# Performance work log

Hardware: AMD Instinct MI355X
Metric: run time of the kernel (lower is better)

The kernel has to match this reference:

```python
import jax, jax.numpy as jnp
import numpy as np

NUM_HEADS = 12
HEAD_DIM = 64
DIM = 768
ATTN_DIM = 768
SEQ = 4096


def _rotate_half(t):
    # split last dim in halves: (x1, x2) -> (-x2, x1)
    x1, x2 = jnp.split(t, 2, axis=-1)
    return jnp.concatenate([-x2, x1], axis=-1)


def _apply_rope(t, freqs):
    # t: [B,H,L,d], freqs: [1,1,L,d]
    return t * jnp.cos(freqs) + _rotate_half(t) * jnp.sin(freqs)


def setup_inputs() -> dict:
    key = jax.random.key(0)
    ks = jax.random.split(key, 8)
    x = jax.random.normal(ks[0], (1, SEQ, DIM), dtype=jnp.float32)
    # standard rotary frequencies: theta = pos * inv_freq, concatenated twice to head_dim
    inv_freq = 1.0 / (10000.0 ** (jnp.arange(0, HEAD_DIM, 2, dtype=jnp.float32) / HEAD_DIM))
    pos = jnp.arange(SEQ, dtype=jnp.float32)
    ang = pos[:, None] * inv_freq[None, :]                      # [L, d/2]
    rope = jnp.concatenate([ang, ang], axis=-1)[None, None]     # [1,1,L,d]
    s = 0.02
    Wq = jax.random.normal(ks[1], (ATTN_DIM, DIM), dtype=jnp.float32) * s
    Wk = jax.random.normal(ks[2], (ATTN_DIM, DIM), dtype=jnp.float32) * s
    Wv = jax.random.normal(ks[3], (ATTN_DIM, DIM), dtype=jnp.float32) * s
    Wo = jax.random.normal(ks[4], (DIM, ATTN_DIM), dtype=jnp.float32) * s
    bo = jnp.zeros((DIM,), dtype=jnp.float32)
    gamma = jnp.ones((DIM,), dtype=jnp.float32)
    beta = jnp.zeros((DIM,), dtype=jnp.float32)
    return {"x": x, "Wq": Wq, "Wk": Wk, "Wv": Wv, "Wo": Wo, "bo": bo,
            "gamma": gamma, "beta": beta, "rope": rope}


def reference(x, Wq, Wk, Wv, Wo, bo, gamma, beta, rope):
    B, L, D = x.shape
    residual = x
    # pre-LayerNorm
    mu = jnp.mean(x, axis=-1, keepdims=True)
    var = jnp.mean((x - mu) ** 2, axis=-1, keepdims=True)
    xn = (x - mu) * jax.lax.rsqrt(var + 1e-5) * gamma + beta

    def heads(t):  # [B,L,attn_dim] -> [B,H,L,d]
        return t.reshape(B, L, NUM_HEADS, HEAD_DIM).transpose(0, 2, 1, 3)

    q = heads(xn @ Wq.T)
    k = heads(xn @ Wk.T)
    v = heads(xn @ Wv.T)
    q = _apply_rope(q, rope)
    k = _apply_rope(k, rope)
    v = _apply_rope(v, rope)

    scale = HEAD_DIM ** -0.5
    dots = jnp.einsum('bhid,bhjd->bhij', q, k) * scale
    # causal mask: positions j > i masked
    i = jnp.arange(L)
    mask = i[:, None] < i[None, :]  # True where future
    neg = -jnp.finfo(dots.dtype).max
    dots = jnp.where(mask[None, None], neg, dots)
    attn_map = jax.nn.softmax(dots, axis=-1)

    o = jnp.einsum('bhij,bhjd->bhid', attn_map, v)
    o = o.transpose(0, 2, 1, 3).reshape(B, L, ATTN_DIM)
    out = o @ Wo.T + bo + residual
    return out, attn_map, dots
```

## Files before the change

### kernel.cpp

```cpp
#include <hip/hip_runtime.h>
#include <hip/hip_bf16.h>
#include <cfloat>
#include <cmath>

#define SEQ 4096
#define DIM 768
#define NH 12
#define HD 64
#define NEG_MASK (-0x1.FEp+127f)

typedef __attribute__((ext_vector_type(8))) short short8_t;
typedef __attribute__((ext_vector_type(4))) float f32x4;

static __device__ __forceinline__ unsigned short f2bf(float f) {
  __hip_bfloat16 h = __float2bfloat16(f);
  unsigned short u;
  __builtin_memcpy(&u, &h, 2);
  return u;
}

__global__ __launch_bounds__(256) void ln_kernel(const float* __restrict__ x,
    const float* __restrict__ gamma, const float* __restrict__ beta,
    unsigned short* __restrict__ xnb) {
  int row = blockIdx.x;
  const float* xr = x + (size_t)row * DIM;
  int t = threadIdx.x;
  float v0 = xr[t], v1 = xr[t + 256], v2 = xr[t + 512];
  float s = v0 + v1 + v2;
  float s2 = v0 * v0 + v1 * v1 + v2 * v2;
  for (int off = 32; off > 0; off >>= 1) {
    s += __shfl_down(s, off, 64);
    s2 += __shfl_down(s2, off, 64);
  }
  __shared__ float red[2][4];
  int wid = t >> 6;
  if ((t & 63) == 0) { red[0][wid] = s; red[1][wid] = s2; }
  __syncthreads();
  s = red[0][0] + red[0][1] + red[0][2] + red[0][3];
  s2 = red[1][0] + red[1][1] + red[1][2] + red[1][3];
  float mu = s * (1.0f / DIM);
  float var = s2 * (1.0f / DIM) - mu * mu;
  float rstd = rsqrtf(var + 1e-5f);
  unsigned short* xo = xnb + (size_t)row * DIM;
  xo[t]       = f2bf((v0 - mu) * rstd * gamma[t]       + beta[t]);
  xo[t + 256] = f2bf((v1 - mu) * rstd * gamma[t + 256] + beta[t + 256]);
  xo[t + 512] = f2bf((v2 - mu) * rstd * gamma[t + 512] + beta[t + 512]);
}

__global__ __launch_bounds__(256) void wcvt_kernel(const float* __restrict__ w0,
    const float* __restrict__ w1, const float* __restrict__ w2, const float* __restrict__ w3,
    unsigned short* __restrict__ o0, unsigned short* __restrict__ o1,
    unsigned short* __restrict__ o2, unsigned short* __restrict__ o3) {
  const float* src; unsigned short* dst;
  switch (blockIdx.y) {
    case 0: src = w0; dst = o0; break;
    case 1: src = w1; dst = o1; break;
    case 2: src = w2; dst = o2; break;
    default: src = w3; dst = o3; break;
  }
  size_t base = ((size_t)blockIdx.x * 256 + threadIdx.x) * 8;
  float4 a = *(const float4*)(src + base);
  float4 b = *(const float4*)(src + base + 4);
  ushort4 ua, ub;
  ua.x = f2bf(a.x); ua.y = f2bf(a.y); ua.z = f2bf(a.z); ua.w = f2bf(a.w);
  ub.x = f2bf(b.x); ub.y = f2bf(b.y); ub.z = f2bf(b.z); ub.w = f2bf(b.w);
  *(ushort4*)(dst + base) = ua;
  *(ushort4*)(dst + base + 4) = ub;
}

__global__ __launch_bounds__(256) void qkv_kernel(const unsigned short* __restrict__ xnb,
    const unsigned short* __restrict__ wqb, const unsigned short* __restrict__ wkb,
    const unsigned short* __restrict__ wvb, const float* __restrict__ ropes,
    unsigned short* __restrict__ qb, unsigned short* __restrict__ kb,
    unsigned short* __restrict__ vbT) {
  int z = blockIdx.z;
  const unsigned short* W = (z == 0) ? wqb : (z == 1) ? wkb : wvb;
  int h = blockIdx.y;
  int n0 = h * 64;
  int tid = threadIdx.x;
  int w = tid >> 6, l = tid & 63;
  int col_l = l & 15, rowg = l >> 4, kgrp = rowg * 8;
  int mbase = blockIdx.x * 64 + w * 16;

  f32x4 acc[4];
  #pragma unroll
  for (int g = 0; g < 4; g++) acc[g] = (f32x4){0.f, 0.f, 0.f, 0.f};

  for (int k0 = 0; k0 < DIM; k0 += 32) {
    short8_t a = *(const short8_t*)(xnb + (size_t)(mbase + col_l) * DIM + k0 + kgrp);
    #pragma unroll
    for (int g = 0; g < 4; g++) {
      short8_t bw = *(const short8_t*)(W + (size_t)(n0 + g * 16 + col_l) * DIM + k0 + kgrp);
      acc[g] = __builtin_amdgcn_mfma_f32_16x16x32_bf16(a, bw, acc[g], 0, 0, 0);
    }
  }

  float res[4][4];
  #pragma unroll
  for (int g = 0; g < 4; g++) {
    int d = g * 16 + col_l;
    #pragma unroll
    for (int r = 0; r < 4; r++) {
      int m = mbase + rowg * 4 + r;
      float f = ropes[(size_t)m * HD + d];
      float val = acc[g][r];
      float oth = acc[g ^ 2][r];
      float rot = (g < 2) ? -oth : oth;
      res[g][r] = val * cosf(f) + rot * sinf(f);
    }
  }

  if (z < 2) {
    unsigned short* dst = (z == 0) ? qb : kb;
    #pragma unroll
    for (int g = 0; g < 4; g++) {
      int d = g * 16 + col_l;
      #pragma unroll
      for (int r = 0; r < 4; r++)
        dst[((size_t)h * SEQ + mbase + rowg * 4 + r) * HD + d] = f2bf(res[g][r]);
    }
  } else {
    #pragma unroll
    for (int g = 0; g < 4; g++) {
      int d = g * 16 + col_l;
      ushort4 u;
      u.x = f2bf(res[g][0]); u.y = f2bf(res[g][1]);
      u.z = f2bf(res[g][2]); u.w = f2bf(res[g][3]);
      *(ushort4*)(vbT + ((size_t)h * HD + d) * SEQ + mbase + rowg * 4) = u;
    }
  }
}

__global__ __launch_bounds__(256) void attn_fused(
    const unsigned short* __restrict__ qb, const unsigned short* __restrict__ kb,
    const unsigned short* __restrict__ vbT,
    float* __restrict__ dots, float* __restrict__ attnp, unsigned short* __restrict__ ob) {
  int band = blockIdx.x;
  int h = blockIdx.y;
  int i0 = band * 16;
  int jd = i0 >> 6;
  int tid = threadIdx.x;
  int w = tid >> 6, l = tid & 63;
  int col_l = l & 15, rg = l >> 4, kgrp = rg * 8;
  int c4 = col_l * 4;

  const unsigned short* qh = qb + (size_t)h * SEQ * HD;
  const unsigned short* kh = kb + (size_t)h * SEQ * HD;
  const unsigned short* vh = vbT + (size_t)h * HD * SEQ;
  size_t obase = (size_t)h * SEQ * SEQ;

  __shared__ float pt[4][16][68];
  __shared__ float stats[4][16][2];

  const unsigned short* qrow = qh + (size_t)(i0 + col_l) * HD + kgrp;
  short8_t aq0 = *(const short8_t*)(qrow);
  short8_t aq1 = *(const short8_t*)(qrow + 32);

  float mreg[4], lreg[4];
  #pragma unroll
  for (int r = 0; r < 4; r++) { mreg[r] = -FLT_MAX; lreg[r] = 0.f; }

  short8_t ka0[4], ka1[4];
  if (w <= jd) {
    #pragma unroll
    for (int b = 0; b < 4; b++) {
      const unsigned short* kr = kh + (size_t)(w * 64 + b * 16 + col_l) * HD + kgrp;
      ka0[b] = *(const short8_t*)(kr);
      ka1[b] = *(const short8_t*)(kr + 32);
    }
  }
  for (int jt = w; jt <= jd; jt += 4) {
    int j0 = jt * 64;
    bool hasNext = (jt + 4 <= jd);
    short8_t kb0[4], kb1[4];
    if (hasNext) {
      #pragma unroll
      for (int b = 0; b < 4; b++) {
        const unsigned short* kr = kh + (size_t)(j0 + 256 + b * 16 + col_l) * HD + kgrp;
        kb0[b] = *(const short8_t*)(kr);
        kb1[b] = *(const short8_t*)(kr + 32);
      }
    }
    f32x4 acc[4];
    #pragma unroll
    for (int b = 0; b < 4; b++) {
      f32x4 z = {0.f, 0.f, 0.f, 0.f};
      acc[b] = __builtin_amdgcn_mfma_f32_16x16x32_bf16(aq0, ka0[b], z, 0, 0, 0);
      acc[b] = __builtin_amdgcn_mfma_f32_16x16x32_bf16(aq1, ka1[b], acc[b], 0, 0, 0);
    }
    bool diag = (jt == jd);
    #pragma unroll
    for (int b = 0; b < 4; b++) {
      int j = j0 + b * 16 + col_l;
      #pragma unroll
      for (int r = 0; r < 4; r++) {
        float s = acc[b][r] * 0.125f;
        acc[b][r] = (diag && j > i0 + rg * 4 + r) ? NEG_MASK : s;
      }
    }
    #pragma unroll
    for (int r = 0; r < 4; r++) {
      float tm = fmaxf(fmaxf(acc[0][r], acc[1][r]), fmaxf(acc[2][r], acc[3][r]));
      if (tm > -1e30f) {
        float nm = fmaxf(mreg[r], tm);
        lreg[r] = lreg[r] * __expf(mreg[r] - nm) +
                  __expf(acc[0][r] - nm) + __expf(acc[1][r] - nm) +
                  __expf(acc[2][r] - nm) + __expf(acc[3][r] - nm);
        mreg[r] = nm;
      }
    }
    #pragma unroll
    for (int b = 0; b < 4; b++)
      #pragma unroll
      for (int r = 0; r < 4; r++)
        pt[w][rg * 4 + r][b * 16 + col_l] = acc[b][r];
    #pragma unroll
    for (int e = 0; e < 4; e++) {
      float4 v = *(const float4*)&pt[w][e * 4 + rg][c4];
      *(float4*)(dots + obase + (size_t)(i0 + e * 4 + rg) * SEQ + j0 + c4) = v;
    }
    if (hasNext) {
      #pragma unroll
      for (int b = 0; b < 4; b++) { ka0[b] = kb0[b]; ka1[b] = kb1[b]; }
    }
  }

  #pragma unroll
  for (int r = 0; r < 4; r++) {
    float m = mreg[r], lv = lreg[r];
    #pragma unroll
    for (int off = 1; off < 16; off <<= 1) {
      float om = __shfl_xor(m, off, 16);
      float ol = __shfl_xor(lv, off, 16);
      float nm = fmaxf(m, om);
      lv = lv * __expf(m - nm) + ol * __expf(om - nm);
      m = nm;
    }
    mreg[r] = m; lreg[r] = lv;
  }
  if (col_l == 0) {
    #pragma unroll
    for (int r = 0; r < 4; r++) {
      stats[w][rg * 4 + r][0] = mreg[r];
      stats[w][rg * 4 + r][1] = lreg[r];
    }
  }
  __syncthreads();
  float M_[4], rl_[4];
  #pragma unroll
  for (int r = 0; r < 4; r++) {
    int row = rg * 4 + r;
    float m0 = stats[0][row][0], m1 = stats[1][row][0];
    float m2 = stats[2][row][0], m3 = stats[3][row][0];
    float mm = fmaxf(fmaxf(m0, m1), fmaxf(m2, m3));
    float L = stats[0][row][1] * __expf(m0 - mm) + stats[1][row][1] * __expf(m1 - mm) +
              stats[2][row][1] * __expf(m2 - mm) + stats[3][row][1] * __expf(m3 - mm);
    M_[r] = mm;
    rl_[r] = 1.0f / L;
  }

  f32x4 o[4];
  #pragma unroll
  for (int dg = 0; dg < 4; dg++) o[dg] = (f32x4){0.f, 0.f, 0.f, 0.f};

  for (int jt = w; jt <= jd; jt += 4) {
    int j0 = jt * 64;
    short8_t bv0[4], bv1[4];
    #pragma unroll
    for (int dg = 0; dg < 4; dg++) {
      const unsigned short* vr = vh + (size_t)(dg * 16 + col_l) * SEQ + j0 + kgrp;
      bv0[dg] = *(const short8_t*)(vr);
      bv1[dg] = *(const short8_t*)(vr + 32);
    }
    f32x4 acc[4];
    #pragma unroll
    for (int b = 0; b < 4; b++) {
      const unsigned short* kr = kh + (size_t)(j0 + b * 16 + col_l) * HD + kgrp;
      short8_t bk0 = *(const short8_t*)(kr);
      short8_t bk1 = *(const short8_t*)(kr + 32);
      f32x4 z = {0.f, 0.f, 0.f, 0.f};
      acc[b] = __builtin_amdgcn_mfma_f32_16x16x32_bf16(aq0, bk0, z, 0, 0, 0);
      acc[b] = __builtin_amdgcn_mfma_f32_16x16x32_bf16(aq1, bk1, acc[b], 0, 0, 0);
    }
    bool diag = (jt == jd);
    #pragma unroll
    for (int b = 0; b < 4; b++) {
      int j = j0 + b * 16 + col_l;
      #pragma unroll
      for (int r = 0; r < 4; r++) {
        float s = acc[b][r] * 0.125f;
        s = (diag && j > i0 + rg * 4 + r) ? NEG_MASK : s;
        float p = __expf(s - M_[r]) * rl_[r];
        pt[w][rg * 4 + r][b * 16 + col_l] = p;
      }
    }
    #pragma unroll
    for (int e = 0; e < 4; e++) {
      float4 v = *(const float4*)&pt[w][e * 4 + rg][c4];
      *(float4*)(attnp + obase + (size_t)(i0 + e * 4 + rg) * SEQ + j0 + c4) = v;
    }
    short8_t pa[2];
    #pragma unroll
    for (int ks = 0; ks < 2; ks++) {
      const float* src = &pt[w][col_l][ks * 32 + kgrp];
      float4 x0 = *(const float4*)src;
      float4 x1 = *(const float4*)(src + 4);
      short8_t t;
      t[0] = (short)f2bf(x0.x); t[1] = (short)f2bf(x0.y);
      t[2] = (short)f2bf(x0.z); t[3] = (short)f2bf(x0.w);
      t[4] = (short)f2bf(x1.x); t[5] = (short)f2bf(x1.y);
      t[6] = (short)f2bf(x1.z); t[7] = (short)f2bf(x1.w);
      pa[ks] = t;
    }
    #pragma unroll
    for (int dg = 0; dg < 4; dg++) {
      o[dg] = __builtin_amdgcn_mfma_f32_16x16x32_bf16(pa[0], bv0[dg], o[dg], 0, 0, 0);
      o[dg] = __builtin_amdgcn_mfma_f32_16x16x32_bf16(pa[1], bv1[dg], o[dg], 0, 0, 0);
    }
  }

  {
    int c0 = (jd + 1) * 64;
    int nf4 = (SEQ - c0) >> 2;
    if (nf4 > 0) {
      float4 dm = make_float4(NEG_MASK, NEG_MASK, NEG_MASK, NEG_MASK);
      float4 zz = make_float4(0.f, 0.f, 0.f, 0.f);
      for (int r16 = 0; r16 < 16; r16++) {
        float4* dr = (float4*)(dots  + obase + (size_t)(i0 + r16) * SEQ + c0);
        float4* ar = (float4*)(attnp + obase + (size_t)(i0 + r16) * SEQ + c0);
        for (int c = tid; c < nf4; c += 256) { dr[c] = dm; ar[c] = zz; }
      }
    }
  }

  __syncthreads();
  #pragma unroll
  for (int dg = 0; dg < 4; dg++)
    #pragma unroll
    for (int r = 0; r < 4; r++)
      pt[w][rg * 4 + r][dg * 16 + col_l] = o[dg][r];
  __syncthreads();
  {
    int idx = tid * 4;
    int row = idx >> 6, col = idx & 63;
    float4 s = *(const float4*)&pt[0][row][col];
    #pragma unroll
    for (int w2 = 1; w2 < 4; w2++) {
      float4 t = *(const float4*)&pt[w2][row][col];
      s.x += t.x; s.y += t.y; s.z += t.z; s.w += t.w;
    }
    ushort4 u;
    u.x = f2bf(s.x); u.y = f2bf(s.y); u.z = f2bf(s.z); u.w = f2bf(s.w);
    *(ushort4*)(ob + (size_t)(i0 + row) * DIM + h * HD + col) = u;
  }
}

__global__ __launch_bounds__(256) void out_kernel(const unsigned short* __restrict__ ob,
    const unsigned short* __restrict__ wob, const float* __restrict__ bias,
    const float* __restrict__ resid, float* __restrict__ out) {
  int n0 = blockIdx.y * 64;
  int tid = threadIdx.x;
  int w = tid >> 6, l = tid & 63;
  int col_l = l & 15, rowg = l >> 4, kgrp = rowg * 8;
  int mbase = blockIdx.x * 64 + w * 16;

  f32x4 acc[4];
  #pragma unroll
  for (int g = 0; g < 4; g++) acc[g] = (f32x4){0.f, 0.f, 0.f, 0.f};

  for (int k0 = 0; k0 < DIM; k0 += 32) {
    short8_t a = *(const short8_t*)(ob + (size_t)(mbase + col_l) * DIM + k0 + kgrp);
    #pragma unroll
    for (int g = 0; g < 4; g++) {
      short8_t bw = *(const short8_t*)(wob + (size_t)(n0 + g * 16 + col_l) * DIM + k0 + kgrp);
      acc[g] = __builtin_amdgcn_mfma_f32_16x16x32_bf16(a, bw, acc[g], 0, 0, 0);
    }
  }
  #pragma unroll
  for (int g = 0; g < 4; g++) {
    int n = n0 + g * 16 + col_l;
    float bn = bias[n];
    #pragma unroll
    for (int r = 0; r < 4; r++) {
      int m = mbase + rowg * 4 + r;
      out[(size_t)m * DIM + n] = acc[g][r] + bn + resid[(size_t)m * DIM + n];
    }
  }
}

extern "C" void kernel_launch(void* const* d_in, const int* in_sizes, int n_in,
                              void* d_out, int out_size, void* d_ws, size_t ws_size,
                              hipStream_t stream) {
  const float* x     = (const float*)d_in[0];
  const float* Wq    = (const float*)d_in[1];
  const float* Wk    = (const float*)d_in[2];
  const float* Wv    = (const float*)d_in[3];
  const float* Wo    = (const float*)d_in[4];
  const float* bo    = (const float*)d_in[5];
  const float* gamma = (const float*)d_in[6];
  const float* beta  = (const float*)d_in[7];
  const float* rope  = (const float*)d_in[8];

  float* out  = (float*)d_out;
  float* attn = out + (size_t)SEQ * DIM;
  float* dots = attn + (size_t)NH * SEQ * SEQ;

  char* ws = (char*)d_ws;
  unsigned short* xnb = (unsigned short*)(ws);
  unsigned short* qb  = (unsigned short*)(ws + 6291456);
  unsigned short* kb  = (unsigned short*)(ws + 12582912);
  unsigned short* vbT = (unsigned short*)(ws + 18874368);
  unsigned short* ob  = (unsigned short*)(ws + 25165824);
  unsigned short* wqb = (unsigned short*)(ws + 31457280);
  unsigned short* wkb = (unsigned short*)(ws + 32636928);
  unsigned short* wvb = (unsigned short*)(ws + 33816576);
  unsigned short* wob = (unsigned short*)(ws + 34996224);

  ln_kernel<<<SEQ, 256, 0, stream>>>(x, gamma, beta, xnb);
  wcvt_kernel<<<dim3(288, 4), 256, 0, stream>>>(Wq, Wk, Wv, Wo, wqb, wkb, wvb, wob);
  qkv_kernel<<<dim3(SEQ / 64, NH, 3), 256, 0, stream>>>(xnb, wqb, wkb, wvb, rope, qb, kb, vbT);
  attn_fused<<<dim3(SEQ / 16, NH), 256, 0, stream>>>(qb, kb, vbT, dots, attn, ob);
  out_kernel<<<dim3(SEQ / 64, DIM / 64), 256, 0, stream>>>(ob, wob, bo, x, out);
}
```

Before: 594.4 us.

## Use nontemporal stores for attention outputs, reverse band order, drop K/V prefetch

```diff
diff --git a/kernel.cpp b/kernel.cpp
--- a/kernel.cpp
+++ b/kernel.cpp
@@ -17,6 +17,13 @@
   unsigned short u;
   __builtin_memcpy(&u, &h, 2);
   return u;
+}
+
+static __device__ __forceinline__ void st_nt(float* p, f32x4 v) {
+  __builtin_nontemporal_store(v, (f32x4*)p);
+}
+static __device__ __forceinline__ f32x4 ld_lds4(const float* p) {
+  return *(const f32x4*)p;
 }
 
 __global__ __launch_bounds__(256) void ln_kernel(const float* __restrict__ x,
@@ -131,11 +138,11 @@
   }
 }
 
-__global__ __launch_bounds__(256) void attn_fused(
+__global__ __launch_bounds__(256, 4) void attn_fused(
     const unsigned short* __restrict__ qb, const unsigned short* __restrict__ kb,
     const unsigned short* __restrict__ vbT,
     float* __restrict__ dots, float* __restrict__ attnp, unsigned short* __restrict__ ob) {
-  int band = blockIdx.x;
+  int band = (SEQ / 16 - 1) - blockIdx.x;
   int h = blockIdx.y;
   int i0 = band * 16;
   int jd = i0 >> 6;
@@ -160,33 +167,17 @@
   #pragma unroll
   for (int r = 0; r < 4; r++) { mreg[r] = -FLT_MAX; lreg[r] = 0.f; }
 
-  short8_t ka0[4], ka1[4];
-  if (w <= jd) {
-    #pragma unroll
-    for (int b = 0; b < 4; b++) {
-      const unsigned short* kr = kh + (size_t)(w * 64 + b * 16 + col_l) * HD + kgrp;
-      ka0[b] = *(const short8_t*)(kr);
-      ka1[b] = *(const short8_t*)(kr + 32);
-    }
-  }
   for (int jt = w; jt <= jd; jt += 4) {
     int j0 = jt * 64;
-    bool hasNext = (jt + 4 <= jd);
-    short8_t kb0[4], kb1[4];
-    if (hasNext) {
-      #pragma unroll
-      for (int b = 0; b < 4; b++) {
-        const unsigned short* kr = kh + (size_t)(j0 + 256 + b * 16 + col_l) * HD + kgrp;
-        kb0[b] = *(const short8_t*)(kr);
-        kb1[b] = *(const short8_t*)(kr + 32);
-      }
-    }
     f32x4 acc[4];
     #pragma unroll
     for (int b = 0; b < 4; b++) {
+      const unsigned short* kr = kh + (size_t)(j0 + b * 16 + col_l) * HD + kgrp;
+      short8_t bk0 = *(const short8_t*)(kr);
+      short8_t bk1 = *(const short8_t*)(kr + 32);
       f32x4 z = {0.f, 0.f, 0.f, 0.f};
-      acc[b] = __builtin_amdgcn_mfma_f32_16x16x32_bf16(aq0, ka0[b], z, 0, 0, 0);
-      acc[b] = __builtin_amdgcn_mfma_f32_16x16x32_bf16(aq1, ka1[b], acc[b], 0, 0, 0);
+      acc[b] = __builtin_amdgcn_mfma_f32_16x16x32_bf16(aq0, bk0, z, 0, 0, 0);
+      acc[b] = __builtin_amdgcn_mfma_f32_16x16x32_bf16(aq1, bk1, acc[b], 0, 0, 0);
     }
     bool diag = (jt == jd);
     #pragma unroll
@@ -216,12 +207,8 @@
         pt[w][rg * 4 + r][b * 16 + col_l] = acc[b][r];
     #pragma unroll
     for (int e = 0; e < 4; e++) {
-      float4 v = *(const float4*)&pt[w][e * 4 + rg][c4];
-      *(float4*)(dots + obase + (size_t)(i0 + e * 4 + rg) * SEQ + j0 + c4) = v;
-    }
-    if (hasNext) {
-      #pragma unroll
-      for (int b = 0; b < 4; b++) { ka0[b] = kb0[b]; ka1[b] = kb1[b]; }
+      f32x4 v = ld_lds4(&pt[w][e * 4 + rg][c4]);
+      st_nt(dots + obase + (size_t)(i0 + e * 4 + rg) * SEQ + j0 + c4, v);
     }
   }
 
@@ -265,13 +252,6 @@
 
   for (int jt = w; jt <= jd; jt += 4) {
     int j0 = jt * 64;
-    short8_t bv0[4], bv1[4];
-    #pragma unroll
-    for (int dg = 0; dg < 4; dg++) {
-      const unsigned short* vr = vh + (size_t)(dg * 16 + col_l) * SEQ + j0 + kgrp;
-      bv0[dg] = *(const short8_t*)(vr);
-      bv1[dg] = *(const short8_t*)(vr + 32);
-    }
     f32x4 acc[4];
     #pragma unroll
     for (int b = 0; b < 4; b++) {
@@ -296,15 +276,15 @@
     }
     #pragma unroll
     for (int e = 0; e < 4; e++) {
-      float4 v = *(const float4*)&pt[w][e * 4 + rg][c4];
-      *(float4*)(attnp + obase + (size_t)(i0 + e * 4 + rg) * SEQ + j0 + c4) = v;
+      f32x4 v = ld_lds4(&pt[w][e * 4 + rg][c4]);
+      st_nt(attnp + obase + (size_t)(i0 + e * 4 + rg) * SEQ + j0 + c4, v);
     }
     short8_t pa[2];
     #pragma unroll
     for (int ks = 0; ks < 2; ks++) {
       const float* src = &pt[w][col_l][ks * 32 + kgrp];
-      float4 x0 = *(const float4*)src;
-      float4 x1 = *(const float4*)(src + 4);
+      f32x4 x0 = ld_lds4(src);
+      f32x4 x1 = ld_lds4(src + 4);
       short8_t t;
       t[0] = (short)f2bf(x0.x); t[1] = (short)f2bf(x0.y);
       t[2] = (short)f2bf(x0.z); t[3] = (short)f2bf(x0.w);
@@ -314,8 +294,11 @@
     }
     #pragma unroll
     for (int dg = 0; dg < 4; dg++) {
-      o[dg] = __builtin_amdgcn_mfma_f32_16x16x32_bf16(pa[0], bv0[dg], o[dg], 0, 0, 0);
-      o[dg] = __builtin_amdgcn_mfma_f32_16x16x32_bf16(pa[1], bv1[dg], o[dg], 0, 0, 0);
+      const unsigned short* vr = vh + (size_t)(dg * 16 + col_l) * SEQ + j0 + kgrp;
+      short8_t bv0 = *(const short8_t*)(vr);
+      short8_t bv1 = *(const short8_t*)(vr + 32);
+      o[dg] = __builtin_amdgcn_mfma_f32_16x16x32_bf16(pa[0], bv0, o[dg], 0, 0, 0);
+      o[dg] = __builtin_amdgcn_mfma_f32_16x16x32_bf16(pa[1], bv1, o[dg], 0, 0, 0);
     }
   }
 
@@ -323,12 +306,15 @@
     int c0 = (jd + 1) * 64;
     int nf4 = (SEQ - c0) >> 2;
     if (nf4 > 0) {
-      float4 dm = make_float4(NEG_MASK, NEG_MASK, NEG_MASK, NEG_MASK);
-      float4 zz = make_float4(0.f, 0.f, 0.f, 0.f);
+      f32x4 dm = (f32x4){NEG_MASK, NEG_MASK, NEG_MASK, NEG_MASK};
+      f32x4 zz = (f32x4){0.f, 0.f, 0.f, 0.f};
       for (int r16 = 0; r16 < 16; r16++) {
-        float4* dr = (float4*)(dots  + obase + (size_t)(i0 + r16) * SEQ + c0);
-        float4* ar = (float4*)(attnp + obase + (size_t)(i0 + r16) * SEQ + c0);
-        for (int c = tid; c < nf4; c += 256) { dr[c] = dm; ar[c] = zz; }
+        float* dr = dots  + obase + (size_t)(i0 + r16) * SEQ + c0;
+        float* ar = attnp + obase + (size_t)(i0 + r16) * SEQ + c0;
+        for (int c = tid; c < nf4; c += 256) {
+          st_nt(dr + c * 4, dm);
+          st_nt(ar + c * 4, zz);
+        }
       }
     }
   }
@@ -343,10 +329,10 @@
   {
     int idx = tid * 4;
     int row = idx >> 6, col = idx & 63;
-    float4 s = *(const float4*)&pt[0][row][col];
+    f32x4 s = ld_lds4(&pt[0][row][col]);
     #pragma unroll
     for (int w2 = 1; w2 < 4; w2++) {
-      float4 t = *(const float4*)&pt[w2][row][col];
+      f32x4 t = ld_lds4(&pt[w2][row][col]);
       s.x += t.x; s.y += t.y; s.z += t.z; s.w += t.w;
     }
     ushort4 u;
```

Measured after the change: 563.7 us. 5.2% less time.
